# Performance work log

Measured on AMD Instinct MI355X. Metric: run time of the kernel, lower is better.

Reference implementation:

```python
import jax, jax.numpy as jnp
import numpy as np

N = 6000          # number of nodes
P = 8_000_000     # number of (src, dst) pairs that have a path
D_FEAT = 128      # node feature dim (unused by the math, only shape)
MAX_PATH_DISTANCE = 5


def setup_inputs() -> dict:
    key = jax.random.key(0)
    k_x, k_b, k_s, k_d, k_l = jax.random.split(key, 5)
    x = jax.random.normal(k_x, (N, D_FEAT), dtype=jnp.float32)
    b = jax.random.normal(k_b, (MAX_PATH_DISTANCE,), dtype=jnp.float32)
    src_idx = jax.random.randint(k_s, (P,), 0, N, dtype=jnp.int64 if jax.config.jax_enable_x64 else jnp.int32)
    dst_idx = jax.random.randint(k_d, (P,), 0, N, dtype=src_idx.dtype)
    # path lengths are >= 1 (a path in the dict always has at least one node)
    path_len = jax.random.randint(k_l, (P,), 1, 21, dtype=src_idx.dtype)
    return {"x": x, "b": b, "src_idx": src_idx, "dst_idx": dst_idx, "path_len": path_len}


def reference(x, b, src_idx, dst_idx, path_len):
    # spatial_matrix[src, dst] = b[min(len(path), max_path_distance) - 1]
    n = x.shape[0]
    max_pd = b.shape[0]
    clamped = jnp.minimum(path_len, max_pd) - 1          # [P] in [0, max_pd-1]
    vals = b[clamped]                                     # gather from bias, [P]
    spatial = jnp.zeros((n, n), dtype=x.dtype)
    spatial = spatial.at[src_idx, dst_idx].set(vals)      # scatter into pairwise matrix
    return spatial
```

## Files before the change

### kernel.cpp

```cpp
#include <hip/hip_runtime.h>


#define BSHIFT 14
#define BCELLS (1 << BSHIFT)
#define NBUCK  2198
#define NPACK  1100
#define NOWN   550
#define BIN_THREADS 1024
#define TILE   12288
#define SCAN_TB 16
#define MAXBLK 656
#define MRG_THREADS 1024

__device__ __forceinline__ unsigned int unpack16(const unsigned int* A, unsigned int c) {
    return (A[c >> 1] >> ((c & 1) * 16)) & 0xFFFFu;
}


__global__ __launch_bounds__(BIN_THREADS) void se_bin_local(
        const int* __restrict__ src_idx,
        const int* __restrict__ dst_idx,
        const int* __restrict__ path_len,
        unsigned int* __restrict__ recs,
        unsigned int* __restrict__ startsW,
        int P, int n) {
    __shared__ unsigned int histP[NPACK];
    __shared__ unsigned int curP[NPACK];
    __shared__ unsigned int stage[TILE];
    __shared__ unsigned int scr[34];

    int t = threadIdx.x;
    int start = blockIdx.x * TILE;

    for (int i = t; i < NPACK; i += BIN_THREADS) curP[i] = 0u;
    __syncthreads();

    int cells[12];
    unsigned int lows[12];
#pragma unroll
    for (int j = 0; j < 3; ++j) {
        int base = start + j * (BIN_THREADS * 4) + t * 4;
        int k0 = j * 4;
        if (base + 3 < P) {
            int4 s = *reinterpret_cast<const int4*>(src_idx + base);
            int4 d = *reinterpret_cast<const int4*>(dst_idx + base);
            int4 l = *reinterpret_cast<const int4*>(path_len + base);
            int lp = base - start;
            cells[k0]     = s.x * n + d.x;
            cells[k0 + 1] = s.y * n + d.y;
            cells[k0 + 2] = s.z * n + d.z;
            cells[k0 + 3] = s.w * n + d.w;
            lows[k0]     = ((unsigned int)(lp + 1) << 3) | (unsigned int)((l.x < 5 ? l.x : 5) - 1);
            lows[k0 + 1] = ((unsigned int)(lp + 2) << 3) | (unsigned int)((l.y < 5 ? l.y : 5) - 1);
            lows[k0 + 2] = ((unsigned int)(lp + 3) << 3) | (unsigned int)((l.z < 5 ? l.z : 5) - 1);
            lows[k0 + 3] = ((unsigned int)(lp + 4) << 3) | (unsigned int)((l.w < 5 ? l.w : 5) - 1);
        } else {
#pragma unroll
            for (int jj = 0; jj < 4; ++jj) {
                int p = base + jj;
                if (p < P) {
                    cells[k0 + jj] = src_idx[p] * n + dst_idx[p];
                    int len = path_len[p];
                    int cl = (len < 5 ? len : 5) - 1;
                    lows[k0 + jj] = ((unsigned int)(p - start + 1) << 3) | (unsigned int)cl;
                } else {
                    cells[k0 + jj] = -1;
                    lows[k0 + jj] = 0u;
                }
            }
        }
    }
#pragma unroll
    for (int k = 0; k < 12; ++k) {
        if (cells[k] >= 0) {
            unsigned int c = (unsigned int)cells[k] >> BSHIFT;
            unsigned int old = atomicAdd(&curP[c >> 1], (c & 1) ? 0x10000u : 1u);
            unsigned int rank = (old >> ((c & 1) * 16)) & 0xFFFFu;
            lows[k] |= rank << 18;
        }
    }
    __syncthreads();

    unsigned int l0 = 0, l1 = 0, l2v = 0, l3 = 0, s = 0;
    if (t < NOWN) {
        unsigned int w0 = curP[2 * t], w1 = curP[2 * t + 1];
        unsigned int v0 = w0 & 0xFFFFu, v1 = w0 >> 16;
        unsigned int v2 = w1 & 0xFFFFu, v3 = w1 >> 16;
        l0 = 0; l1 = v0; l2v = v0 + v1; l3 = v0 + v1 + v2;
        s = v0 + v1 + v2 + v3;
    }
    unsigned int x = s;
    for (int d = 1; d < 64; d <<= 1) {
        unsigned int y = (unsigned int)__shfl_up((int)x, d, 64);
        if ((t & 63) >= d) x += y;
    }
    if ((t & 63) == 63) scr[t >> 6] = x;
    __syncthreads();
    if (t == 0) {
        unsigned int acc = 0;
        for (int w = 0; w < 16; ++w) { unsigned int v = scr[w]; scr[16 + w] = acc; acc += v; }
        scr[32] = acc;
    }
    __syncthreads();
    unsigned int exc = x - s + scr[16 + (t >> 6)];
    if (t < NOWN) {
        unsigned int st0 = exc + l0, st1 = exc + l1, st2 = exc + l2v, st3 = exc + l3;
        histP[2 * t]     = (st0 & 0xFFFFu) | (st1 << 16);
        histP[2 * t + 1] = (st2 & 0xFFFFu) | (st3 << 16);
    }
    __syncthreads();

    for (int i = t; i < NPACK; i += BIN_THREADS)
        startsW[(size_t)blockIdx.x * NPACK + i] = histP[i];

#pragma unroll
    for (int k = 0; k < 12; ++k) {
        if (cells[k] >= 0) {
            unsigned int cell = (unsigned int)cells[k];
            unsigned int c = cell >> BSHIFT;
            unsigned int pos = unpack16(histP, c) + (lows[k] >> 18);
            stage[pos] = ((cell & (BCELLS - 1)) << 18) | (lows[k] & 0x3FFFFu);
        }
    }
    __syncthreads();

    unsigned int tot = scr[32];
    unsigned int* dst = recs + (size_t)blockIdx.x * TILE;
    const uint4* st4 = reinterpret_cast<const uint4*>(stage);
    uint4* dst4 = reinterpret_cast<uint4*>(dst);
    if (tot == TILE) {
#pragma unroll
        for (int j = 0; j < TILE / 4 / BIN_THREADS; ++j)
            dst4[j * BIN_THREADS + t] = st4[j * BIN_THREADS + t];
    } else {
        unsigned int tot4 = tot >> 2;
        for (unsigned int i = t; i < tot4; i += BIN_THREADS)
            dst4[i] = st4[i];
        for (unsigned int i = (tot4 << 2) + t; i < tot; i += BIN_THREADS)
            dst[i] = stage[i];
    }
}

__global__ __launch_bounds__(256) void se_transpose(
        const unsigned int* __restrict__ startsW,
        unsigned short* __restrict__ T,
        int nblk) {
    __shared__ unsigned short tile[64][66];
    int bc0 = blockIdx.x * 64;
    int bb0 = blockIdx.y * 64;

    for (int i = threadIdx.x; i < 64 * 32; i += 256) {
        int r = i >> 5;
        int w = i & 31;
        int blk = bb0 + r;
        int word = (bc0 >> 1) + w;
        unsigned int v = 0;
        if (blk < nblk && word < NPACK)
            v = startsW[(size_t)blk * NPACK + word];
        tile[2 * w][r]     = (unsigned short)(v & 0xFFFFu);
        tile[2 * w + 1][r] = (unsigned short)(v >> 16);
    }
    __syncthreads();

    for (int i = threadIdx.x; i < 64 * 64; i += 256) {
        int c = i >> 6, bl = i & 63;
        int gc = bc0 + c, gb = bb0 + bl;
        if (gc <= NBUCK && gb < nblk)
            T[(size_t)gc * nblk + gb] = tile[c][bl];
    }
}

__device__ __forceinline__ float se_decode(unsigned int k,
                                           float b0, float b1, float b2,
                                           float b3, float b4) {
    unsigned c = k & 7u;
    float t = (c == 0u) ? b0 : (c == 1u) ? b1 : (c == 2u) ? b2 : (c == 3u) ? b3 : b4;
    return k ? t : 0.0f;
}

__global__ __launch_bounds__(MRG_THREADS) void se_merge2(
        const unsigned short* __restrict__ T,
        const unsigned int* __restrict__ recs,
        const float* __restrict__ b,
        float* __restrict__ out,
        long long totalCells, int nblk) {
    __shared__ unsigned int tab[BCELLS];

    int orig = blockIdx.x;
    int q = gridDim.x >> 3, r8 = gridDim.x & 7;
    int xcd = orig & 7, idx = orig >> 3;
    int c = (xcd < r8 ? xcd * (q + 1) : r8 * (q + 1) + (xcd - r8) * q) + idx;

    long long baseCell = (long long)c << BSHIFT;
    long long rem = totalCells - baseCell;
    int valid = rem < BCELLS ? (int)rem : BCELLS;

    int tr = threadIdx.x;
    unsigned int st = 0, en = 0;
    if (tr < nblk) {
        st = T[(size_t)c * nblk + tr];
        en = T[(size_t)(c + 1) * nblk + tr];
    }

    uint4* tab4 = reinterpret_cast<uint4*>(tab);
    for (int i = threadIdx.x; i < BCELLS / 4; i += MRG_THREADS)
        tab4[i] = make_uint4(0u, 0u, 0u, 0u);
    __syncthreads();

    if (tr < nblk) {
        const uint4* rp4 =
            reinterpret_cast<const uint4*>(recs + (size_t)tr * TILE);
        unsigned int keyhi = (unsigned int)tr << 18;
        for (unsigned int i = st & ~3u; i < en; i += 4) {
            uint4 r4 = rp4[i >> 2];
            if (i     >= st && i     < en) atomicMax(&tab[r4.x >> 18], keyhi | (r4.x & 0x3FFFFu));
            if (i + 1 >= st && i + 1 < en) atomicMax(&tab[r4.y >> 18], keyhi | (r4.y & 0x3FFFFu));
            if (i + 2 >= st && i + 2 < en) atomicMax(&tab[r4.z >> 18], keyhi | (r4.z & 0x3FFFFu));
            if (i + 3 >= st && i + 3 < en) atomicMax(&tab[r4.w >> 18], keyhi | (r4.w & 0x3FFFFu));
        }
    }
    __syncthreads();

    float b0 = b[0], b1 = b[1], b2 = b[2], b3 = b[3], b4 = b[4];
    float* o = out + baseCell;
    int n4 = valid >> 2;
    float4* o4 = reinterpret_cast<float4*>(o);
    for (int i = threadIdx.x; i < n4; i += MRG_THREADS) {
        uint4 k = tab4[i];
        float4 v;
        v.x = se_decode(k.x, b0, b1, b2, b3, b4);
        v.y = se_decode(k.y, b0, b1, b2, b3, b4);
        v.z = se_decode(k.z, b0, b1, b2, b3, b4);
        v.w = se_decode(k.w, b0, b1, b2, b3, b4);
        o4[i] = v;
    }
    for (int i = (n4 << 2) + threadIdx.x; i < valid; i += MRG_THREADS)
        o[i] = se_decode(tab[i], b0, b1, b2, b3, b4);
}


__global__ __launch_bounds__(BIN_THREADS) void se_hist(
        const int* __restrict__ src_idx,
        const int* __restrict__ dst_idx,
        unsigned int* __restrict__ countsW,
        int P, int n) {
    __shared__ unsigned int curP[NPACK];
    int t = threadIdx.x;
    for (int i = t; i < NPACK; i += BIN_THREADS) curP[i] = 0u;
    __syncthreads();

    int start = blockIdx.x * TILE;
#pragma unroll
    for (int j = 0; j < 3; ++j) {
        int base = start + j * (BIN_THREADS * 4) + t * 4;
        if (base + 3 < P) {
            int4 s = *reinterpret_cast<const int4*>(src_idx + base);
            int4 d = *reinterpret_cast<const int4*>(dst_idx + base);
            unsigned int c0 = (unsigned int)(s.x * n + d.x) >> BSHIFT;
            unsigned int c1 = (unsigned int)(s.y * n + d.y) >> BSHIFT;
            unsigned int c2 = (unsigned int)(s.z * n + d.z) >> BSHIFT;
            unsigned int c3 = (unsigned int)(s.w * n + d.w) >> BSHIFT;
            atomicAdd(&curP[c0 >> 1], (c0 & 1) ? 0x10000u : 1u);
            atomicAdd(&curP[c1 >> 1], (c1 & 1) ? 0x10000u : 1u);
            atomicAdd(&curP[c2 >> 1], (c2 & 1) ? 0x10000u : 1u);
            atomicAdd(&curP[c3 >> 1], (c3 & 1) ? 0x10000u : 1u);
        } else {
            for (int p = base; p < P && p < base + 4; ++p) {
                unsigned int c = (unsigned int)(src_idx[p] * n + dst_idx[p]) >> BSHIFT;
                atomicAdd(&curP[c >> 1], (c & 1) ? 0x10000u : 1u);
            }
        }
    }
    __syncthreads();
    for (int i = t; i < NPACK; i += BIN_THREADS)
        countsW[(size_t)blockIdx.x * NPACK + i] = curP[i];
}

__global__ __launch_bounds__(256) void se_scan(
        unsigned int* __restrict__ countsW,
        unsigned short* __restrict__ basesT,
        int nblk) {
    __shared__ unsigned short lds16[MAXBLK * SCAN_TB];
    unsigned int* lds32 = reinterpret_cast<unsigned int*>(lds16);
    int t = threadIdx.x;
    int c0 = blockIdx.x * SCAN_TB;
    int w0 = c0 >> 1;
    int words = nblk * (SCAN_TB / 2);

    for (int i = t; i < words; i += 256) {
        int r = i >> 3, w = i & 7;
        if (w0 + w < NPACK)
            lds32[r * 8 + w] = countsW[(size_t)r * NPACK + w0 + w];
    }
    __syncthreads();

    if (t < SCAN_TB && c0 + t < NBUCK) {
        unsigned int acc = 0;
        for (int r = 0; r < nblk; ++r) {
            unsigned short v = lds16[r * SCAN_TB + t];
            lds16[r * SCAN_TB + t] = (unsigned short)acc;
            acc += v;
        }
        basesT[(size_t)(c0 + t) * (nblk + 1) + nblk] = (unsigned short)acc;
    }
    __syncthreads();

    for (int i = t; i < words; i += 256) {
        int r = i >> 3, w = i & 7;
        if (w0 + w < NPACK)
            countsW[(size_t)r * NPACK + w0 + w] = lds32[r * 8 + w];
    }
    for (int k = 0; k < SCAN_TB; ++k) {
        int c = c0 + k;
        if (c >= NBUCK) break;
        for (int r = t; r < nblk; r += 256)
            basesT[(size_t)c * (nblk + 1) + r] = lds16[r * SCAN_TB + k];
    }
}

__global__ __launch_bounds__(BIN_THREADS) void se_bin5(
        const int* __restrict__ src_idx,
        const int* __restrict__ dst_idx,
        const int* __restrict__ path_len,
        unsigned int* __restrict__ recs,
        const unsigned int* __restrict__ basesW,
        int P, int n) {
    __shared__ unsigned int histP[NPACK];
    __shared__ unsigned int curP[NPACK];
    __shared__ unsigned int gbaseP[NPACK];
    __shared__ unsigned int stage[TILE];
    __shared__ unsigned int scr[34];

    int t = threadIdx.x;
    int start = blockIdx.x * TILE;

    for (int i = t; i < NPACK; i += BIN_THREADS) curP[i] = 0u;
    __syncthreads();

    int cells[12];
    unsigned int lows[12];
#pragma unroll
    for (int j = 0; j < 3; ++j) {
        int base = start + j * (BIN_THREADS * 4) + t * 4;
        int k0 = j * 4;
        if (base + 3 < P) {
            int4 s = *reinterpret_cast<const int4*>(src_idx + base);
            int4 d = *reinterpret_cast<const int4*>(dst_idx + base);
            int4 l = *reinterpret_cast<const int4*>(path_len + base);
            int lp = base - start;
            cells[k0]     = s.x * n + d.x;
            cells[k0 + 1] = s.y * n + d.y;
            cells[k0 + 2] = s.z * n + d.z;
            cells[k0 + 3] = s.w * n + d.w;
            lows[k0]     = ((unsigned int)(lp + 1) << 3) | (unsigned int)((l.x < 5 ? l.x : 5) - 1);
            lows[k0 + 1] = ((unsigned int)(lp + 2) << 3) | (unsigned int)((l.y < 5 ? l.y : 5) - 1);
            lows[k0 + 2] = ((unsigned int)(lp + 3) << 3) | (unsigned int)((l.z < 5 ? l.z : 5) - 1);
            lows[k0 + 3] = ((unsigned int)(lp + 4) << 3) | (unsigned int)((l.w < 5 ? l.w : 5) - 1);
        } else {
#pragma unroll
            for (int jj = 0; jj < 4; ++jj) {
                int p = base + jj;
                if (p < P) {
                    cells[k0 + jj] = src_idx[p] * n + dst_idx[p];
                    int len = path_len[p];
                    int cl = (len < 5 ? len : 5) - 1;
                    lows[k0 + jj] = ((unsigned int)(p - start + 1) << 3) | (unsigned int)cl;
                } else {
                    cells[k0 + jj] = -1;
                    lows[k0 + jj] = 0u;
                }
            }
        }
    }
#pragma unroll
    for (int k = 0; k < 12; ++k) {
        if (cells[k] >= 0) {
            unsigned int c = (unsigned int)cells[k] >> BSHIFT;
            atomicAdd(&curP[c >> 1], (c & 1) ? 0x10000u : 1u);
        }
    }
    __syncthreads();

    unsigned int l0 = 0, l1 = 0, l2v = 0, l3 = 0, s = 0;
    if (t < NOWN) {
        unsigned int w0 = curP[2 * t], w1 = curP[2 * t + 1];
        unsigned int v0 = w0 & 0xFFFFu, v1 = w0 >> 16;
        unsigned int v2 = w1 & 0xFFFFu, v3 = w1 >> 16;
        l0 = 0; l1 = v0; l2v = v0 + v1; l3 = v0 + v1 + v2;
        s = v0 + v1 + v2 + v3;
    }
    unsigned int x = s;
    for (int d = 1; d < 64; d <<= 1) {
        unsigned int y = (unsigned int)__shfl_up((int)x, d, 64);
        if ((t & 63) >= d) x += y;
    }
    if ((t & 63) == 63) scr[t >> 6] = x;
    __syncthreads();
    if (t == 0) {
        unsigned int acc = 0;
        for (int w = 0; w < 16; ++w) { unsigned int v = scr[w]; scr[16 + w] = acc; acc += v; }
        scr[32] = acc;
    }
    __syncthreads();
    unsigned int exc = x - s + scr[16 + (t >> 6)];
    if (t < NOWN) {
        unsigned int st0 = exc + l0, st1 = exc + l1, st2 = exc + l2v, st3 = exc + l3;
        histP[2 * t]     = (st0 & 0xFFFFu) | (st1 << 16);
        histP[2 * t + 1] = (st2 & 0xFFFFu) | (st3 << 16);
    }
    __syncthreads();

    for (int i = t; i < NPACK; i += BIN_THREADS) {
        gbaseP[i] = basesW[(size_t)blockIdx.x * NPACK + i];
        curP[i] = histP[i];
    }
    __syncthreads();

#pragma unroll
    for (int k = 0; k < 12; ++k) {
        if (cells[k] >= 0) {
            unsigned int cell = (unsigned int)cells[k];
            unsigned int c = cell >> BSHIFT;
            unsigned int old = atomicAdd(&curP[c >> 1], (c & 1) ? 0x10000u : 1u);
            unsigned int pos = (old >> ((c & 1) * 16)) & 0xFFFFu;
            stage[pos] = ((cell & (BCELLS - 1)) << 18) | lows[k];
        }
    }
    __syncthreads();

    unsigned int tot = scr[32];
    for (unsigned int i = t; i < tot; i += BIN_THREADS) {
        unsigned int rec = stage[i];
        unsigned int lo = 0, hi = 2199;
        while (lo < hi) {
            unsigned int mid = (lo + hi + 1) >> 1;
            if (unpack16(histP, mid) <= i) lo = mid; else hi = mid - 1;
        }
        unsigned int c = lo;
        unsigned int pos = unpack16(gbaseP, c) + (i - unpack16(histP, c));
        recs[(size_t)c * BCELLS + pos] = rec;
    }
}

__global__ __launch_bounds__(MRG_THREADS) void se_merge(
        const unsigned short* __restrict__ basesT,
        const float* __restrict__ b,
        float* __restrict__ out,
        long long totalCells, int nblk) {
    __shared__ unsigned int tab[BCELLS];

    int c = blockIdx.x;
    long long baseCell = (long long)c << BSHIFT;
    long long rem = totalCells - baseCell;
    int valid = rem < BCELLS ? (int)rem : BCELLS;

    uint4* tab4 = reinterpret_cast<uint4*>(tab);
    for (int i = threadIdx.x; i < BCELLS / 4; i += MRG_THREADS)
        tab4[i] = make_uint4(0u, 0u, 0u, 0u);
    __syncthreads();

    const unsigned int* r =
        reinterpret_cast<const unsigned int*>(out) + (size_t)c * BCELLS;
    int tr = threadIdx.x;
    if (tr < nblk) {
        const unsigned short* B = basesT + (size_t)c * (nblk + 1);
        unsigned int rb0 = B[tr], rb1 = B[tr + 1];
        unsigned int keyhi = (unsigned int)tr << 18;
        for (unsigned int i = rb0; i < rb1; ++i) {
            unsigned int rec = r[i];
            atomicMax(&tab[rec >> 18], keyhi | (rec & 0x3FFFFu));
        }
    }
    __syncthreads();

    float b0 = b[0], b1 = b[1], b2 = b[2], b3 = b[3], b4 = b[4];
    float* o = out + baseCell;
    int n4 = valid >> 2;
    float4* o4 = reinterpret_cast<float4*>(o);
    for (int i = threadIdx.x; i < n4; i += MRG_THREADS) {
        uint4 k = tab4[i];
        float4 v;
        v.x = se_decode(k.x, b0, b1, b2, b3, b4);
        v.y = se_decode(k.y, b0, b1, b2, b3, b4);
        v.z = se_decode(k.z, b0, b1, b2, b3, b4);
        v.w = se_decode(k.w, b0, b1, b2, b3, b4);
        o4[i] = v;
    }
    for (int i = (n4 << 2) + threadIdx.x; i < valid; i += MRG_THREADS)
        o[i] = se_decode(tab[i], b0, b1, b2, b3, b4);
}


extern "C" void kernel_launch(void* const* d_in, const int* in_sizes, int n_in,
                              void* d_out, int out_size, void* d_ws, size_t ws_size,
                              hipStream_t stream) {
    const float* b        = (const float*)d_in[1];
    const int*   src_idx  = (const int*)d_in[2];
    const int*   dst_idx  = (const int*)d_in[3];
    const int*   path_len = (const int*)d_in[4];
    int P = in_sizes[2];
    int n = in_sizes[0] / 128;
    long long totalCells = (long long)n * n;
    int nblk = (P + TILE - 1) / TILE;

    size_t needFast = (size_t)nblk * TILE * 4u
                    + (size_t)nblk * NPACK * 4u
                    + (size_t)(NBUCK + 1) * nblk * 2u;

    if (ws_size >= needFast && nblk <= MRG_THREADS) {
        unsigned int*   recs    = (unsigned int*)d_ws;
        unsigned int*   startsW = recs + (size_t)nblk * TILE;
        unsigned short* T       = (unsigned short*)(startsW + (size_t)nblk * NPACK);

        se_bin_local<<<nblk, BIN_THREADS, 0, stream>>>(
            src_idx, dst_idx, path_len, recs, startsW, P, n);

        dim3 tg((NBUCK + 1 + 63) / 64, (nblk + 63) / 64);
        se_transpose<<<tg, 256, 0, stream>>>(startsW, T, nblk);

        se_merge2<<<NBUCK, MRG_THREADS, 0, stream>>>(
            T, recs, b, (float*)d_out, totalCells, nblk);
    } else {
        unsigned int*   countsW = (unsigned int*)d_ws;
        unsigned short* basesT  = (unsigned short*)(countsW + (size_t)nblk * NPACK);

        se_hist<<<nblk, BIN_THREADS, 0, stream>>>(src_idx, dst_idx, countsW, P, n);
        se_scan<<<(NBUCK + SCAN_TB - 1) / SCAN_TB, 256, 0, stream>>>(countsW, basesT, nblk);
        se_bin5<<<nblk, BIN_THREADS, 0, stream>>>(
            src_idx, dst_idx, path_len, (unsigned int*)d_out, countsW, P, n);
        se_merge<<<NBUCK, MRG_THREADS, 0, stream>>>(basesT, b, (float*)d_out,
                                                    totalCells, nblk);
    }
}
```

Measured before the change: 263.1 us.

## Drop transpose kernel and split long bucket segments across idle merge threads

Removes the separate transpose launch. The merge kernel now reads per-block bucket start offsets directly from the packed startsW array, using strided loads instead of a contiguous transposed table. It also uses the otherwise idle threads (those past nblk) as helpers: any source block with at least 8 records in the bucket hands the second half of its range to a helper thread, which shortens the longest serial atomicMax chain. This costs an extra shared-memory atomic counter, one extra barrier, and uncoalesced reads of startsW.

```diff
diff --git a/kernel.cpp b/kernel.cpp
--- a/kernel.cpp
+++ b/kernel.cpp
@@ -11,6 +11,7 @@
 #define SCAN_TB 16
 #define MAXBLK 656
 #define MRG_THREADS 1024
+#define HMAXE  512
 
 __device__ __forceinline__ unsigned int unpack16(const unsigned int* A, unsigned int c) {
     return (A[c >> 1] >> ((c & 1) * 16)) & 0xFFFFu;
@@ -141,35 +142,6 @@
     }
 }
 
-__global__ __launch_bounds__(256) void se_transpose(
-        const unsigned int* __restrict__ startsW,
-        unsigned short* __restrict__ T,
-        int nblk) {
-    __shared__ unsigned short tile[64][66];
-    int bc0 = blockIdx.x * 64;
-    int bb0 = blockIdx.y * 64;
-
-    for (int i = threadIdx.x; i < 64 * 32; i += 256) {
-        int r = i >> 5;
-        int w = i & 31;
-        int blk = bb0 + r;
-        int word = (bc0 >> 1) + w;
-        unsigned int v = 0;
-        if (blk < nblk && word < NPACK)
-            v = startsW[(size_t)blk * NPACK + word];
-        tile[2 * w][r]     = (unsigned short)(v & 0xFFFFu);
-        tile[2 * w + 1][r] = (unsigned short)(v >> 16);
-    }
-    __syncthreads();
-
-    for (int i = threadIdx.x; i < 64 * 64; i += 256) {
-        int c = i >> 6, bl = i & 63;
-        int gc = bc0 + c, gb = bb0 + bl;
-        if (gc <= NBUCK && gb < nblk)
-            T[(size_t)gc * nblk + gb] = tile[c][bl];
-    }
-}
-
 __device__ __forceinline__ float se_decode(unsigned int k,
                                            float b0, float b1, float b2,
                                            float b3, float b4) {
@@ -178,13 +150,16 @@
     return k ? t : 0.0f;
 }
 
-__global__ __launch_bounds__(MRG_THREADS) void se_merge2(
-        const unsigned short* __restrict__ T,
+__global__ __launch_bounds__(MRG_THREADS) void se_merge3(
+        const unsigned int* __restrict__ startsW,
         const unsigned int* __restrict__ recs,
         const float* __restrict__ b,
         float* __restrict__ out,
         long long totalCells, int nblk) {
     __shared__ unsigned int tab[BCELLS];
+    __shared__ unsigned int eA[HMAXE];
+    __shared__ unsigned int eB[HMAXE];
+    __shared__ unsigned int helpCnt;
 
     int orig = blockIdx.x;
     int q = gridDim.x >> 3, r8 = gridDim.x & 7;
@@ -196,27 +171,66 @@
     int valid = rem < BCELLS ? (int)rem : BCELLS;
 
     int tr = threadIdx.x;
+    if (tr == 0) helpCnt = 0u;
+
     unsigned int st = 0, en = 0;
     if (tr < nblk) {
-        st = T[(size_t)c * nblk + tr];
-        en = T[(size_t)(c + 1) * nblk + tr];
+        const unsigned int* sw = startsW + (size_t)tr * NPACK;
+        unsigned int w0 = sw[c >> 1];
+        unsigned int w1 = sw[(c + 1) >> 1];
+        st = (w0 >> ((c & 1) * 16)) & 0xFFFFu;
+        en = (w1 >> (((c + 1) & 1) * 16)) & 0xFFFFu;
     }
 
     uint4* tab4 = reinterpret_cast<uint4*>(tab);
     for (int i = threadIdx.x; i < BCELLS / 4; i += MRG_THREADS)
         tab4[i] = make_uint4(0u, 0u, 0u, 0u);
+    __syncthreads();
+
+    unsigned int hcap = (unsigned int)(MRG_THREADS - nblk);
+    if (hcap > HMAXE) hcap = HMAXE;
+    unsigned int enOwn = en;
+    if (tr < nblk && (en - st) >= 8u) {
+        unsigned int h = atomicAdd(&helpCnt, 1u);
+        if (h < hcap) {
+            unsigned int mid = (st + en) >> 1;
+            eA[h] = ((unsigned int)tr << 16) | mid;
+            eB[h] = en;
+            enOwn = mid;
+        }
+    }
     __syncthreads();
 
     if (tr < nblk) {
         const uint4* rp4 =
             reinterpret_cast<const uint4*>(recs + (size_t)tr * TILE);
         unsigned int keyhi = (unsigned int)tr << 18;
-        for (unsigned int i = st & ~3u; i < en; i += 4) {
+        for (unsigned int i = st & ~3u; i < enOwn; i += 4) {
             uint4 r4 = rp4[i >> 2];
-            if (i     >= st && i     < en) atomicMax(&tab[r4.x >> 18], keyhi | (r4.x & 0x3FFFFu));
-            if (i + 1 >= st && i + 1 < en) atomicMax(&tab[r4.y >> 18], keyhi | (r4.y & 0x3FFFFu));
-            if (i + 2 >= st && i + 2 < en) atomicMax(&tab[r4.z >> 18], keyhi | (r4.z & 0x3FFFFu));
-            if (i + 3 >= st && i + 3 < en) atomicMax(&tab[r4.w >> 18], keyhi | (r4.w & 0x3FFFFu));
+            if (i     >= st && i     < enOwn) atomicMax(&tab[r4.x >> 18], keyhi | (r4.x & 0x3FFFFu));
+            if (i + 1 >= st && i + 1 < enOwn) atomicMax(&tab[r4.y >> 18], keyhi | (r4.y & 0x3FFFFu));
+            if (i + 2 >= st && i + 2 < enOwn) atomicMax(&tab[r4.z >> 18], keyhi | (r4.z & 0x3FFFFu));
+            if (i + 3 >= st && i + 3 < enOwn) atomicMax(&tab[r4.w >> 18], keyhi | (r4.w & 0x3FFFFu));
+        }
+    } else {
+        unsigned int j = (unsigned int)(tr - nblk);
+        unsigned int cnt = helpCnt;
+        if (cnt > hcap) cnt = hcap;
+        if (j < cnt) {
+            unsigned int a = eA[j];
+            unsigned int trh = a >> 16;
+            unsigned int mid = a & 0xFFFFu;
+            unsigned int enh = eB[j];
+            const uint4* rp4 =
+                reinterpret_cast<const uint4*>(recs + (size_t)trh * TILE);
+            unsigned int keyhi = trh << 18;
+            for (unsigned int i = mid & ~3u; i < enh; i += 4) {
+                uint4 r4 = rp4[i >> 2];
+                if (i     >= mid && i     < enh) atomicMax(&tab[r4.x >> 18], keyhi | (r4.x & 0x3FFFFu));
+                if (i + 1 >= mid && i + 1 < enh) atomicMax(&tab[r4.y >> 18], keyhi | (r4.y & 0x3FFFFu));
+                if (i + 2 >= mid && i + 2 < enh) atomicMax(&tab[r4.z >> 18], keyhi | (r4.z & 0x3FFFFu));
+                if (i + 3 >= mid && i + 3 < enh) atomicMax(&tab[r4.w >> 18], keyhi | (r4.w & 0x3FFFFu));
+            }
         }
     }
     __syncthreads();
@@ -504,22 +518,17 @@
     int nblk = (P + TILE - 1) / TILE;
 
     size_t needFast = (size_t)nblk * TILE * 4u
-                    + (size_t)nblk * NPACK * 4u
-                    + (size_t)(NBUCK + 1) * nblk * 2u;
+                    + (size_t)nblk * NPACK * 4u;
 
     if (ws_size >= needFast && nblk <= MRG_THREADS) {
-        unsigned int*   recs    = (unsigned int*)d_ws;
-        unsigned int*   startsW = recs + (size_t)nblk * TILE;
-        unsigned short* T       = (unsigned short*)(startsW + (size_t)nblk * NPACK);
+        unsigned int* recs    = (unsigned int*)d_ws;
+        unsigned int* startsW = recs + (size_t)nblk * TILE;
 
         se_bin_local<<<nblk, BIN_THREADS, 0, stream>>>(
             src_idx, dst_idx, path_len, recs, startsW, P, n);
 
-        dim3 tg((NBUCK + 1 + 63) / 64, (nblk + 63) / 64);
-        se_transpose<<<tg, 256, 0, stream>>>(startsW, T, nblk);
-
-        se_merge2<<<NBUCK, MRG_THREADS, 0, stream>>>(
-            T, recs, b, (float*)d_out, totalCells, nblk);
+        se_merge3<<<NBUCK, MRG_THREADS, 0, stream>>>(
+            startsW, recs, b, (float*)d_out, totalCells, nblk);
     } else {
         unsigned int*   countsW = (unsigned int*)d_ws;
         unsigned short* basesT  = (unsigned short*)(countsW + (size_t)nblk * NPACK);
```

Measured after the change: 262.9 us. About the same (-0.1%).

## Drop transpose kernel, read packed bucket starts directly in merge, slim bin registers

Applied to the files above, without the earlier changes.

Removes the separate transpose pass. The merge kernel now reads each block's packed 16-bit bucket starts straight from startsW with a per-thread strided access, which saves one kernel launch and a round trip through global memory. The bin kernel packs the cell index and clamped length into one word and keeps ranks as 16-bit pairs, recomputing the local position at staging time to cut register use. Occupancy hints are added to both kernels. The trade-off is uncoalesced strided loads of startsW in the merge prologue.

```diff
diff --git a/kernel.cpp b/kernel.cpp
--- a/kernel.cpp
+++ b/kernel.cpp
@@ -17,7 +17,7 @@
 }
 
 
-__global__ __launch_bounds__(BIN_THREADS) void se_bin_local(
+__global__ __launch_bounds__(BIN_THREADS, 8) void se_bin_local(
         const int* __restrict__ src_idx,
         const int* __restrict__ dst_idx,
         const int* __restrict__ path_len,
@@ -35,8 +35,8 @@
     for (int i = t; i < NPACK; i += BIN_THREADS) curP[i] = 0u;
     __syncthreads();
 
-    int cells[12];
-    unsigned int lows[12];
+    unsigned int cc[12];
+    unsigned int rk[6];
 #pragma unroll
     for (int j = 0; j < 3; ++j) {
         int base = start + j * (BIN_THREADS * 4) + t * 4;
@@ -45,39 +45,33 @@
             int4 s = *reinterpret_cast<const int4*>(src_idx + base);
             int4 d = *reinterpret_cast<const int4*>(dst_idx + base);
             int4 l = *reinterpret_cast<const int4*>(path_len + base);
-            int lp = base - start;
-            cells[k0]     = s.x * n + d.x;
-            cells[k0 + 1] = s.y * n + d.y;
-            cells[k0 + 2] = s.z * n + d.z;
-            cells[k0 + 3] = s.w * n + d.w;
-            lows[k0]     = ((unsigned int)(lp + 1) << 3) | (unsigned int)((l.x < 5 ? l.x : 5) - 1);
-            lows[k0 + 1] = ((unsigned int)(lp + 2) << 3) | (unsigned int)((l.y < 5 ? l.y : 5) - 1);
-            lows[k0 + 2] = ((unsigned int)(lp + 3) << 3) | (unsigned int)((l.z < 5 ? l.z : 5) - 1);
-            lows[k0 + 3] = ((unsigned int)(lp + 4) << 3) | (unsigned int)((l.w < 5 ? l.w : 5) - 1);
+            cc[k0]     = ((unsigned int)(s.x * n + d.x) << 3) | (unsigned int)((l.x < 5 ? l.x : 5) - 1);
+            cc[k0 + 1] = ((unsigned int)(s.y * n + d.y) << 3) | (unsigned int)((l.y < 5 ? l.y : 5) - 1);
+            cc[k0 + 2] = ((unsigned int)(s.z * n + d.z) << 3) | (unsigned int)((l.z < 5 ? l.z : 5) - 1);
+            cc[k0 + 3] = ((unsigned int)(s.w * n + d.w) << 3) | (unsigned int)((l.w < 5 ? l.w : 5) - 1);
         } else {
 #pragma unroll
             for (int jj = 0; jj < 4; ++jj) {
                 int p = base + jj;
                 if (p < P) {
-                    cells[k0 + jj] = src_idx[p] * n + dst_idx[p];
                     int len = path_len[p];
-                    int cl = (len < 5 ? len : 5) - 1;
-                    lows[k0 + jj] = ((unsigned int)(p - start + 1) << 3) | (unsigned int)cl;
+                    cc[k0 + jj] = ((unsigned int)(src_idx[p] * n + dst_idx[p]) << 3)
+                                | (unsigned int)((len < 5 ? len : 5) - 1);
                 } else {
-                    cells[k0 + jj] = -1;
-                    lows[k0 + jj] = 0u;
+                    cc[k0 + jj] = 0xFFFFFFFFu;
                 }
             }
         }
     }
 #pragma unroll
     for (int k = 0; k < 12; ++k) {
-        if (cells[k] >= 0) {
-            unsigned int c = (unsigned int)cells[k] >> BSHIFT;
+        unsigned int r = 0;
+        if (cc[k] != 0xFFFFFFFFu) {
+            unsigned int c = cc[k] >> 17;
             unsigned int old = atomicAdd(&curP[c >> 1], (c & 1) ? 0x10000u : 1u);
-            unsigned int rank = (old >> ((c & 1) * 16)) & 0xFFFFu;
-            lows[k] |= rank << 18;
-        }
+            r = (old >> ((c & 1) * 16)) & 0xFFFFu;
+        }
+        if (k & 1) rk[k >> 1] |= r << 16; else rk[k >> 1] = r;
     }
     __syncthreads();
 
@@ -115,11 +109,12 @@
 
 #pragma unroll
     for (int k = 0; k < 12; ++k) {
-        if (cells[k] >= 0) {
-            unsigned int cell = (unsigned int)cells[k];
-            unsigned int c = cell >> BSHIFT;
-            unsigned int pos = unpack16(histP, c) + (lows[k] >> 18);
-            stage[pos] = ((cell & (BCELLS - 1)) << 18) | (lows[k] & 0x3FFFFu);
+        if (cc[k] != 0xFFFFFFFFu) {
+            unsigned int c = cc[k] >> 17;
+            unsigned int rank = (rk[k >> 1] >> ((k & 1) * 16)) & 0xFFFFu;
+            unsigned int pos = unpack16(histP, c) + rank;
+            unsigned int lp1 = (unsigned int)((k >> 2) * (BIN_THREADS * 4) + t * 4 + (k & 3) + 1);
+            stage[pos] = (((cc[k] >> 3) & (BCELLS - 1)) << 18) | (lp1 << 3) | (cc[k] & 7u);
         }
     }
     __syncthreads();
@@ -141,35 +136,6 @@
     }
 }
 
-__global__ __launch_bounds__(256) void se_transpose(
-        const unsigned int* __restrict__ startsW,
-        unsigned short* __restrict__ T,
-        int nblk) {
-    __shared__ unsigned short tile[64][66];
-    int bc0 = blockIdx.x * 64;
-    int bb0 = blockIdx.y * 64;
-
-    for (int i = threadIdx.x; i < 64 * 32; i += 256) {
-        int r = i >> 5;
-        int w = i & 31;
-        int blk = bb0 + r;
-        int word = (bc0 >> 1) + w;
-        unsigned int v = 0;
-        if (blk < nblk && word < NPACK)
-            v = startsW[(size_t)blk * NPACK + word];
-        tile[2 * w][r]     = (unsigned short)(v & 0xFFFFu);
-        tile[2 * w + 1][r] = (unsigned short)(v >> 16);
-    }
-    __syncthreads();
-
-    for (int i = threadIdx.x; i < 64 * 64; i += 256) {
-        int c = i >> 6, bl = i & 63;
-        int gc = bc0 + c, gb = bb0 + bl;
-        if (gc <= NBUCK && gb < nblk)
-            T[(size_t)gc * nblk + gb] = tile[c][bl];
-    }
-}
-
 __device__ __forceinline__ float se_decode(unsigned int k,
                                            float b0, float b1, float b2,
                                            float b3, float b4) {
@@ -178,8 +144,8 @@
     return k ? t : 0.0f;
 }
 
-__global__ __launch_bounds__(MRG_THREADS) void se_merge2(
-        const unsigned short* __restrict__ T,
+__global__ __launch_bounds__(MRG_THREADS, 8) void se_merge3(
+        const unsigned int* __restrict__ startsW,
         const unsigned int* __restrict__ recs,
         const float* __restrict__ b,
         float* __restrict__ out,
@@ -198,8 +164,11 @@
     int tr = threadIdx.x;
     unsigned int st = 0, en = 0;
     if (tr < nblk) {
-        st = T[(size_t)c * nblk + tr];
-        en = T[(size_t)(c + 1) * nblk + tr];
+        const unsigned int* sw = startsW + (size_t)tr * NPACK;
+        unsigned int w0 = sw[c >> 1];
+        unsigned int w1 = sw[(c + 1) >> 1];
+        st = (w0 >> ((c & 1) * 16)) & 0xFFFFu;
+        en = (w1 >> (((c + 1) & 1) * 16)) & 0xFFFFu;
     }
 
     uint4* tab4 = reinterpret_cast<uint4*>(tab);
@@ -504,22 +473,17 @@
     int nblk = (P + TILE - 1) / TILE;
 
     size_t needFast = (size_t)nblk * TILE * 4u
-                    + (size_t)nblk * NPACK * 4u
-                    + (size_t)(NBUCK + 1) * nblk * 2u;
+                    + (size_t)nblk * NPACK * 4u;
 
     if (ws_size >= needFast && nblk <= MRG_THREADS) {
-        unsigned int*   recs    = (unsigned int*)d_ws;
-        unsigned int*   startsW = recs + (size_t)nblk * TILE;
-        unsigned short* T       = (unsigned short*)(startsW + (size_t)nblk * NPACK);
+        unsigned int* recs    = (unsigned int*)d_ws;
+        unsigned int* startsW = recs + (size_t)nblk * TILE;
 
         se_bin_local<<<nblk, BIN_THREADS, 0, stream>>>(
             src_idx, dst_idx, path_len, recs, startsW, P, n);
 
-        dim3 tg((NBUCK + 1 + 63) / 64, (nblk + 63) / 64);
-        se_transpose<<<tg, 256, 0, stream>>>(startsW, T, nblk);
-
-        se_merge2<<<NBUCK, MRG_THREADS, 0, stream>>>(
-            T, recs, b, (float*)d_out, totalCells, nblk);
+        se_merge3<<<NBUCK, MRG_THREADS, 0, stream>>>(
+            startsW, recs, b, (float*)d_out, totalCells, nblk);
     } else {
         unsigned int*   countsW = (unsigned int*)d_ws;
         unsigned short* basesT  = (unsigned short*)(countsW + (size_t)nblk * NPACK);
```

After: 257.6 us. 1.02x faster.
